# Performance work log

Hardware: AMD Instinct MI355X
Metric: run time of the kernel (lower is better)

## Reference

```python
import jax, jax.numpy as jnp
import numpy as np

B, S, D, H = 2, 2048, 1024, 16
DH = D // H  # 64


def setup_inputs() -> dict:
    key = jax.random.key(0)
    ks = jax.random.split(key, 6)
    scale = 1.0 / np.sqrt(D)
    x = jax.random.normal(ks[0], (B, S, D), dtype=jnp.float32)
    Wq = jax.random.normal(ks[1], (D, D), dtype=jnp.float32) * scale
    Wk = jax.random.normal(ks[2], (D, D), dtype=jnp.float32) * scale
    Wv = jax.random.normal(ks[3], (D, D), dtype=jnp.float32) * scale
    Wo = jax.random.normal(ks[4], (D, D), dtype=jnp.float32) * scale
    zeros = jnp.zeros((D,), dtype=jnp.float32)
    return {"x": x, "Wq": Wq, "bq": zeros, "Wk": Wk, "bk": zeros,
            "Wv": Wv, "bv": zeros, "Wo": Wo, "bo": zeros}


def reference(x, Wq, bq, Wk, bk, Wv, bv, Wo, bo):
    # x: [B, S, D]
    def split_heads(t):
        # [B, S, D] -> [B, H, S, DH]
        return t.reshape(B, S, H, DH).transpose(0, 2, 1, 3)

    q = split_heads(x @ Wq + bq)
    k = split_heads(x @ Wk + bk)
    v = split_heads(x @ Wv + bv)

    scores = jnp.einsum('bhqd,bhkd->bhqk', q, k) / jnp.sqrt(jnp.float32(DH))
    weights = jax.nn.softmax(scores, axis=-1)          # [B, H, S, S]
    o = jnp.einsum('bhqk,bhkd->bhqd', weights, v)       # [B, H, S, DH]
    o = o.transpose(0, 2, 1, 3).reshape(B, S, D)        # merge heads
    return o @ Wo + bo
```

## Files before the change

### kernel.cpp

```cpp
#include <hip/hip_runtime.h>
#include <hip/hip_bf16.h>

#define DEV __device__ __forceinline__

typedef short bf16x8 __attribute__((ext_vector_type(8)));
typedef float f32x4 __attribute__((ext_vector_type(4)));
typedef unsigned int u32;

constexpr int BB = 2, SS = 2048, DD = 1024, HH = 16, DHD = 64;
constexpr int MM = BB * SS;
#define QSC 0.1803368801111f

#if __has_builtin(__builtin_amdgcn_exp2f)
#define EXP2(x) __builtin_amdgcn_exp2f(x)
#else
#define EXP2(x) exp2f(x)
#endif

DEV unsigned short f2bf(float f) {
    union { float f; unsigned int u; } v; v.f = f;
    return (unsigned short)((v.u + 0x8000u) >> 16);
}
#if __has_builtin(__builtin_amdgcn_perm)
DEV u32 pk2bf(float a, float b) {
    union { float f; u32 u; } ua, ub; ua.f = a; ub.f = b;
    return __builtin_amdgcn_perm(ub.u + 0x8000u, ua.u + 0x8000u, 0x07060302u);
}
#else
DEV u32 pk2bf(float a, float b) {
    union { float f; u32 u; } ua, ub; ua.f = a; ub.f = b;
    return ((ua.u + 0x8000u) >> 16) | ((ub.u + 0x8000u) & 0xffff0000u);
}
#endif

DEV bf16x8 ld_bf16x8(const unsigned short* p) { return *(const bf16x8*)p; }

DEV void gl16(const unsigned short* g, unsigned short* l) {
    __builtin_amdgcn_global_load_lds(
        (const __attribute__((address_space(1))) u32*)g,
        (__attribute__((address_space(3))) u32*)l, 16, 0, 0);
}

__global__ void prep(const float* __restrict__ x, unsigned short* __restrict__ xb,
                     const float* __restrict__ W0, const float* __restrict__ W1,
                     const float* __restrict__ W2, const float* __restrict__ W3,
                     unsigned short* __restrict__ WtBase) {
    __shared__ float tile[32][33];
    int blk = blockIdx.x;
    if (blk < 4096) {
        int i = blk * 256 + threadIdx.x;
        float4 v = ((const float4*)x)[i];
        uint2 o;
        o.x = pk2bf(v.x, v.y);
        o.y = pk2bf(v.z, v.w);
        ((uint2*)xb)[i] = o;
        return;
    }
    blk -= 4096;
    int wsel = blk >> 10;
    const float* W = (wsel == 0) ? W0 : (wsel == 1) ? W1 : (wsel == 2) ? W2 : W3;
    unsigned short* Wt = WtBase + (size_t)wsel * DD * DD;
    int t = blk & 1023;
    int n0 = (t & 31) * 32, k0 = (t >> 5) * 32;
    int tx = threadIdx.x & 31, ty = threadIdx.x >> 5;
    #pragma unroll
    for (int i = 0; i < 4; ++i)
        tile[ty + 8 * i][tx] = W[(size_t)(k0 + ty + 8 * i) * DD + n0 + tx];
    __syncthreads();
    #pragma unroll
    for (int i = 0; i < 4; ++i)
        Wt[(size_t)(n0 + ty + 8 * i) * DD + k0 + tx] = f2bf(tile[tx][ty + 8 * i]);
}

__global__ __launch_bounds__(256) void qkv_gemm(
    const unsigned short* __restrict__ xb,
    const unsigned short* __restrict__ WtBase,
    const float* __restrict__ bq, const float* __restrict__ bk, const float* __restrict__ bv,
    unsigned short* __restrict__ Qb, unsigned short* __restrict__ Kb, unsigned short* __restrict__ Vt)
{
    __shared__ __align__(16) unsigned short Ald[2][128 * 32];
    __shared__ __align__(16) unsigned short Bld[2][128 * 32];

    const int z = blockIdx.z;
    const unsigned short* Wt = WtBase + (size_t)z * DD * DD;
    const float* bias = (z == 0) ? bq : (z == 1) ? bk : bv;

    const int m0g = blockIdx.y * 128;
    const int n0g = blockIdx.x * 128;
    const int wave = threadIdx.x >> 6, lane = threadIdx.x & 63;
    const int quad = lane >> 4, lcol = lane & 15;
    const int mb = (wave & 1) * 64, nb = (wave >> 1) * 64;

    f32x4 acc[4][4];
    #pragma unroll
    for (int i = 0; i < 4; ++i)
        #pragma unroll
        for (int j = 0; j < 4; ++j) acc[i][j] = (f32x4){0.f, 0.f, 0.f, 0.f};

    auto stage = [&](int ks, int bf) {
        #pragma unroll
        for (int i = 0; i < 4; ++i) {
            int j = wave * 4 + i;
            if (j < 8) {
                int bi = j * 64 + lane;
                int row = bi >> 2, p = (bi & 3) ^ (row & 3);
                gl16(xb + (size_t)(m0g + row) * DD + ks + p * 8, &Ald[bf][j * 512]);
            } else {
                int jj = j - 8;
                int bi = jj * 64 + lane;
                int row = bi >> 2, p = (bi & 3) ^ (row & 3);
                gl16(Wt + (size_t)(n0g + row) * DD + ks + p * 8, &Bld[bf][jj * 512]);
            }
        }
    };

    stage(0, 0);
    __syncthreads();

    for (int kk = 0; kk < 32; ++kk) {
        int bf = kk & 1;
        if (kk + 1 < 32) stage((kk + 1) * 32, (kk + 1) & 1);
        bf16x8 af[4], bfr[4];
        #pragma unroll
        for (int mt = 0; mt < 4; ++mt) {
            int row = mb + mt * 16 + lcol;
            af[mt] = ld_bf16x8(&Ald[bf][(row * 4 + (quad ^ (row & 3))) * 8]);
        }
        #pragma unroll
        for (int nt = 0; nt < 4; ++nt) {
            int row = nb + nt * 16 + lcol;
            bfr[nt] = ld_bf16x8(&Bld[bf][(row * 4 + (quad ^ (row & 3))) * 8]);
        }
        if (z < 2) {
            #pragma unroll
            for (int mt = 0; mt < 4; ++mt)
                #pragma unroll
                for (int nt = 0; nt < 4; ++nt)
                    acc[mt][nt] = __builtin_amdgcn_mfma_f32_16x16x32_bf16(bfr[nt], af[mt], acc[mt][nt], 0, 0, 0);
        } else {
            #pragma unroll
            for (int mt = 0; mt < 4; ++mt)
                #pragma unroll
                for (int nt = 0; nt < 4; ++nt)
                    acc[mt][nt] = __builtin_amdgcn_mfma_f32_16x16x32_bf16(af[mt], bfr[nt], acc[mt][nt], 0, 0, 0);
        }
        __syncthreads();
    }

    if (z < 2) {
        unsigned short* dst = (z == 0) ? Qb : Kb;
        const float sc = (z == 0) ? QSC : 1.0f;
        #pragma unroll
        for (int mt = 0; mt < 4; ++mt)
            #pragma unroll
            for (int nt = 0; nt < 4; ++nt) {
                int m = m0g + mb + mt * 16 + lcol;
                int nbt = n0g + nb + nt * 16 + quad * 4;
                int b = m >> 11, s = m & (SS - 1);
                int h = nbt >> 6, dh0 = nbt & 63;
                float4 bv4 = *(const float4*)&bias[nbt];
                uint2 o;
                o.x = pk2bf((acc[mt][nt][0] + bv4.x) * sc, (acc[mt][nt][1] + bv4.y) * sc);
                o.y = pk2bf((acc[mt][nt][2] + bv4.z) * sc, (acc[mt][nt][3] + bv4.w) * sc);
                *(uint2*)&dst[(((size_t)b * HH + h) * SS + s) * DHD + dh0] = o;
            }
    } else {
        #pragma unroll
        for (int mt = 0; mt < 4; ++mt)
            #pragma unroll
            for (int nt = 0; nt < 4; ++nt) {
                int n = n0g + nb + nt * 16 + lcol;
                int mbt = m0g + mb + mt * 16 + quad * 4;
                int h = n >> 6, dh = n & 63;
                int b = mbt >> 11, s0 = mbt & (SS - 1);
                float bvv = bias[n];
                uint2 o;
                o.x = pk2bf(acc[mt][nt][0] + bvv, acc[mt][nt][1] + bvv);
                o.y = pk2bf(acc[mt][nt][2] + bvv, acc[mt][nt][3] + bvv);
                *(uint2*)&Vt[(((size_t)b * HH + h) * DHD + dh) * SS + s0] = o;
            }
    }
}

__global__ __launch_bounds__(512, 4) void attn(
    const unsigned short* __restrict__ Qb,
    const unsigned short* __restrict__ Kb,
    const unsigned short* __restrict__ Vt,
    unsigned short* __restrict__ Ob)
{
    __shared__ __align__(16) unsigned short Kld[2][64 * 64];
    __shared__ __align__(16) unsigned short Vld[2][64 * 64];
    __shared__ __align__(16) unsigned short tb[8][16 * 68];

    const int g = blockIdx.y * gridDim.x + blockIdx.x;
    const int bh = (g & 7) * 4 + ((g >> 3) & 3);
    const int qt = g >> 5;
    const int b = bh >> 4, h = bh & (HH - 1);
    const unsigned short* Qbh = Qb + (size_t)bh * SS * DHD;
    const unsigned short* Kbh = Kb + (size_t)bh * SS * DHD;
    const unsigned short* Vbh = Vt + (size_t)bh * DHD * SS;

    const int wave = threadIdx.x >> 6, lane = threadIdx.x & 63;
    const int quad = lane >> 4, lcol = lane & 15;
    const int rowbase = qt * 128 + wave * 16;

    bf16x8 qf0 = ld_bf16x8(Qbh + (size_t)(rowbase + lcol) * DHD + quad * 8);
    bf16x8 qf1 = ld_bf16x8(Qbh + (size_t)(rowbase + lcol) * DHD + 32 + quad * 8);

    auto stage = [&](int c, int bf) {
        int kb = c * 64;
        #pragma unroll
        for (int i = 0; i < 2; ++i) {
            int j = wave * 2 + i;
            if (j < 8) {
                int bi = j * 64 + lane;
                int r = bi >> 3, p = (bi & 7) ^ (r & 7);
                gl16(Kbh + (size_t)(kb + r) * DHD + p * 8, &Kld[bf][j * 512]);
            } else {
                int jj = j - 8;
                int bi = jj * 64 + lane;
                int dh = bi >> 3, p = (bi & 7) ^ (dh & 7);
                gl16(Vbh + (size_t)dh * SS + kb + p * 8, &Vld[bf][jj * 512]);
            }
        }
    };

    stage(0, 0);
    __syncthreads();

    float m0 = -1e30f;
    #pragma unroll
    for (int kt = 0; kt < 4; ++kt) {
        int r0 = kt * 16 + lcol;
        bf16x8 ka0 = ld_bf16x8(&Kld[0][(r0 * 8 + (quad ^ (r0 & 7))) * 8]);
        bf16x8 ka1 = ld_bf16x8(&Kld[0][(r0 * 8 + ((quad + 4) ^ (r0 & 7))) * 8]);
        f32x4 s = (f32x4){0.f, 0.f, 0.f, 0.f};
        s = __builtin_amdgcn_mfma_f32_16x16x32_bf16(ka0, qf0, s, 0, 0, 0);
        s = __builtin_amdgcn_mfma_f32_16x16x32_bf16(ka1, qf1, s, 0, 0, 0);
        #pragma unroll
        for (int r = 0; r < 4; ++r) m0 = fmaxf(m0, s[r]);
    }
    #pragma unroll
    for (int msk = 1; msk < 64; msk <<= 1) m0 = fmaxf(m0, __shfl_xor(m0, msk, 64));
    const f32x4 minit = (f32x4){-m0, -m0, -m0, -m0};

    f32x4 oacc[4];
    #pragma unroll
    for (int nt = 0; nt < 4; ++nt) oacc[nt] = (f32x4){0.f, 0.f, 0.f, 0.f};
    float ps = 0.f;

    for (int c = 0; c < 32; ++c) {
        int bf = c & 1;
        if (c + 1 < 32) stage(c + 1, (c + 1) & 1);

        #pragma unroll
        for (int kt = 0; kt < 4; ++kt) {
            int r0 = kt * 16 + lcol;
            bf16x8 ka0 = ld_bf16x8(&Kld[bf][(r0 * 8 + (quad ^ (r0 & 7))) * 8]);
            bf16x8 ka1 = ld_bf16x8(&Kld[bf][(r0 * 8 + ((quad + 4) ^ (r0 & 7))) * 8]);
            f32x4 s = minit;
            s = __builtin_amdgcn_mfma_f32_16x16x32_bf16(ka0, qf0, s, 0, 0, 0);
            s = __builtin_amdgcn_mfma_f32_16x16x32_bf16(ka1, qf1, s, 0, 0, 0);
            float e0 = EXP2(s[0]), e1 = EXP2(s[1]);
            float e2 = EXP2(s[2]), e3 = EXP2(s[3]);
            ps += (e0 + e1) + (e2 + e3);
            *(uint2*)&tb[wave][lcol * 68 + kt * 16 + quad * 4] =
                make_uint2(pk2bf(e0, e1), pk2bf(e2, e3));
        }

        #pragma unroll
        for (int kf2 = 0; kf2 < 2; ++kf2) {
            bf16x8 pa = *(const bf16x8*)&tb[wave][lcol * 68 + kf2 * 32 + quad * 8];
            #pragma unroll
            for (int nt = 0; nt < 4; ++nt) {
                int dh = nt * 16 + lcol;
                bf16x8 vb = ld_bf16x8(&Vld[bf][(dh * 8 + ((kf2 * 4 + quad) ^ (dh & 7))) * 8]);
                oacc[nt] = __builtin_amdgcn_mfma_f32_16x16x32_bf16(pa, vb, oacc[nt], 0, 0, 0);
            }
        }
        __syncthreads();
    }

    ps += __shfl_xor(ps, 16, 64);
    ps += __shfl_xor(ps, 32, 64);
    float inv = 1.0f / ps;
    #pragma unroll
    for (int r = 0; r < 4; ++r) {
        float iv = __shfl(inv, quad * 4 + r, 64);
        int srow = rowbase + quad * 4 + r;
        size_t base = (((size_t)b * SS + srow) * HH + h) * DHD;
        #pragma unroll
        for (int nt = 0; nt < 4; ++nt)
            Ob[base + nt * 16 + lcol] = f2bf(oacc[nt][r] * iv);
    }
}

__global__ __launch_bounds__(256) void out_gemm(
    const unsigned short* __restrict__ Ob,
    const unsigned short* __restrict__ Wto,
    const float* __restrict__ bo,
    float* __restrict__ out)
{
    __shared__ __align__(16) unsigned short Wld[2][128 * 64];
    __shared__ __align__(16) unsigned short Old[2][64 * 64];

    const int m0g = blockIdx.y * 64;
    const int n0g = blockIdx.x * 128;
    const int wave = threadIdx.x >> 6, lane = threadIdx.x & 63;
    const int quad = lane >> 4, lcol = lane & 15;
    const int nb = wave * 32;

    f32x4 acc[2][4];
    #pragma unroll
    for (int i = 0; i < 2; ++i)
        #pragma unroll
        for (int j = 0; j < 4; ++j) acc[i][j] = (f32x4){0.f, 0.f, 0.f, 0.f};

    auto stage = [&](int ks, int bf) {
        #pragma unroll
        for (int i = 0; i < 6; ++i) {
            int j = wave * 6 + i;
            if (j < 16) {
                int bi = j * 64 + lane;
                int r = bi >> 3, p = (bi & 7) ^ (r & 7);
                gl16(Wto + (size_t)(n0g + r) * DD + ks + p * 8, &Wld[bf][j * 512]);
            } else {
                int jj = j - 16;
                int bi = jj * 64 + lane;
                int r = bi >> 3, p = (bi & 7) ^ (r & 7);
                gl16(Ob + (size_t)(m0g + r) * DD + ks + p * 8, &Old[bf][jj * 512]);
            }
        }
    };

    stage(0, 0);
    __syncthreads();

    for (int kk = 0; kk < 16; ++kk) {
        int bf = kk & 1;
        if (kk + 1 < 16) stage((kk + 1) * 64, (kk + 1) & 1);
        #pragma unroll
        for (int kh = 0; kh < 2; ++kh) {
            bf16x8 wf[2], of[4];
            #pragma unroll
            for (int i = 0; i < 2; ++i) {
                int row = nb + i * 16 + lcol;
                wf[i] = ld_bf16x8(&Wld[bf][(row * 8 + ((kh * 4 + quad) ^ (row & 7))) * 8]);
            }
            #pragma unroll
            for (int j = 0; j < 4; ++j) {
                int row = j * 16 + lcol;
                of[j] = ld_bf16x8(&Old[bf][(row * 8 + ((kh * 4 + quad) ^ (row & 7))) * 8]);
            }
            #pragma unroll
            for (int i = 0; i < 2; ++i)
                #pragma unroll
                for (int j = 0; j < 4; ++j)
                    acc[i][j] = __builtin_amdgcn_mfma_f32_16x16x32_bf16(wf[i], of[j], acc[i][j], 0, 0, 0);
        }
        __syncthreads();
    }

    #pragma unroll
    for (int i = 0; i < 2; ++i) {
        int n4 = n0g + nb + i * 16 + quad * 4;
        float4 bv4 = *(const float4*)&bo[n4];
        #pragma unroll
        for (int j = 0; j < 4; ++j) {
            int token = m0g + j * 16 + lcol;
            float4 o;
            o.x = acc[i][j][0] + bv4.x;
            o.y = acc[i][j][1] + bv4.y;
            o.z = acc[i][j][2] + bv4.z;
            o.w = acc[i][j][3] + bv4.w;
            *(float4*)&out[(size_t)token * DD + n4] = o;
        }
    }
}

extern "C" void kernel_launch(void* const* d_in, const int* in_sizes, int n_in,
                              void* d_out, int out_size, void* d_ws, size_t ws_size,
                              hipStream_t stream)
{
    const float* x  = (const float*)d_in[0];
    const float* Wq = (const float*)d_in[1];
    const float* bq = (const float*)d_in[2];
    const float* Wk = (const float*)d_in[3];
    const float* bk = (const float*)d_in[4];
    const float* Wv = (const float*)d_in[5];
    const float* bv = (const float*)d_in[6];
    const float* Wo = (const float*)d_in[7];
    const float* bo = (const float*)d_in[8];
    float* out = (float*)d_out;

    unsigned short* ws = (unsigned short*)d_ws;
    unsigned short* Wt  = ws;
    unsigned short* Wto = Wt + 3 * (size_t)DD * DD;
    unsigned short* Qb  = Wt + 4 * (size_t)DD * DD;
    unsigned short* Kb  = Qb + (size_t)MM * DD;
    unsigned short* Vt  = Kb + (size_t)MM * DD;
    unsigned short* xb  = Vt + (size_t)MM * DD;
    unsigned short* Ob  = xb;

    prep<<<8192, 256, 0, stream>>>(x, xb, Wq, Wk, Wv, Wo, Wt);

    qkv_gemm<<<dim3(DD / 128, MM / 128, 3), 256, 0, stream>>>(xb, Wt, bq, bk, bv, Qb, Kb, Vt);

    attn<<<dim3(16, 32), 512, 0, stream>>>(Qb, Kb, Vt, Ob);

    out_gemm<<<dim3(DD / 128, MM / 64), 256, 0, stream>>>(Ob, Wto, bo, out);
}
```

Measured before the change: 204.3 us.

## Give each attention wave two query row groups to reuse K/V fragments

```diff
diff --git a/kernel.cpp b/kernel.cpp
--- a/kernel.cpp
+++ b/kernel.cpp
@@ -32,6 +32,12 @@
     return ((ua.u + 0x8000u) >> 16) | ((ub.u + 0x8000u) & 0xffff0000u);
 }
 #endif
+
+DEV u32 cvtpk2bf(float a, float b) {
+    u32 r;
+    asm("v_cvt_pk_bf16_f32 %0, %1, %2" : "=v"(r) : "v"(a), "v"(b));
+    return r;
+}
 
 DEV bf16x8 ld_bf16x8(const unsigned short* p) { return *(const bf16x8*)p; }
 
@@ -182,7 +188,7 @@
     }
 }
 
-__global__ __launch_bounds__(512, 4) void attn(
+__global__ __launch_bounds__(256) void attn(
     const unsigned short* __restrict__ Qb,
     const unsigned short* __restrict__ Kb,
     const unsigned short* __restrict__ Vt,
@@ -190,7 +196,7 @@
 {
     __shared__ __align__(16) unsigned short Kld[2][64 * 64];
     __shared__ __align__(16) unsigned short Vld[2][64 * 64];
-    __shared__ __align__(16) unsigned short tb[8][16 * 68];
+    __shared__ __align__(16) unsigned short tb[4][32 * 68];
 
     const int g = blockIdx.y * gridDim.x + blockIdx.x;
     const int bh = (g & 7) * 4 + ((g >> 3) & 3);
@@ -202,16 +208,20 @@
 
     const int wave = threadIdx.x >> 6, lane = threadIdx.x & 63;
     const int quad = lane >> 4, lcol = lane & 15;
-    const int rowbase = qt * 128 + wave * 16;
-
-    bf16x8 qf0 = ld_bf16x8(Qbh + (size_t)(rowbase + lcol) * DHD + quad * 8);
-    bf16x8 qf1 = ld_bf16x8(Qbh + (size_t)(rowbase + lcol) * DHD + 32 + quad * 8);
+    const int rowbase = qt * 128 + wave * 32;
+
+    bf16x8 qf0[2], qf1[2];
+    #pragma unroll
+    for (int gq = 0; gq < 2; ++gq) {
+        qf0[gq] = ld_bf16x8(Qbh + (size_t)(rowbase + gq * 16 + lcol) * DHD + quad * 8);
+        qf1[gq] = ld_bf16x8(Qbh + (size_t)(rowbase + gq * 16 + lcol) * DHD + 32 + quad * 8);
+    }
 
     auto stage = [&](int c, int bf) {
         int kb = c * 64;
         #pragma unroll
-        for (int i = 0; i < 2; ++i) {
-            int j = wave * 2 + i;
+        for (int i = 0; i < 4; ++i) {
+            int j = wave * 4 + i;
             if (j < 8) {
                 int bi = j * 64 + lane;
                 int r = bi >> 3, p = (bi & 7) ^ (r & 7);
@@ -234,20 +244,25 @@
         int r0 = kt * 16 + lcol;
         bf16x8 ka0 = ld_bf16x8(&Kld[0][(r0 * 8 + (quad ^ (r0 & 7))) * 8]);
         bf16x8 ka1 = ld_bf16x8(&Kld[0][(r0 * 8 + ((quad + 4) ^ (r0 & 7))) * 8]);
-        f32x4 s = (f32x4){0.f, 0.f, 0.f, 0.f};
-        s = __builtin_amdgcn_mfma_f32_16x16x32_bf16(ka0, qf0, s, 0, 0, 0);
-        s = __builtin_amdgcn_mfma_f32_16x16x32_bf16(ka1, qf1, s, 0, 0, 0);
-        #pragma unroll
-        for (int r = 0; r < 4; ++r) m0 = fmaxf(m0, s[r]);
+        #pragma unroll
+        for (int gq = 0; gq < 2; ++gq) {
+            f32x4 s = (f32x4){0.f, 0.f, 0.f, 0.f};
+            s = __builtin_amdgcn_mfma_f32_16x16x32_bf16(ka0, qf0[gq], s, 0, 0, 0);
+            s = __builtin_amdgcn_mfma_f32_16x16x32_bf16(ka1, qf1[gq], s, 0, 0, 0);
+            #pragma unroll
+            for (int r = 0; r < 4; ++r) m0 = fmaxf(m0, s[r]);
+        }
     }
     #pragma unroll
     for (int msk = 1; msk < 64; msk <<= 1) m0 = fmaxf(m0, __shfl_xor(m0, msk, 64));
     const f32x4 minit = (f32x4){-m0, -m0, -m0, -m0};
 
-    f32x4 oacc[4];
-    #pragma unroll
-    for (int nt = 0; nt < 4; ++nt) oacc[nt] = (f32x4){0.f, 0.f, 0.f, 0.f};
-    float ps = 0.f;
+    f32x4 oacc[2][4];
+    #pragma unroll
+    for (int gq = 0; gq < 2; ++gq)
+        #pragma unroll
+        for (int nt = 0; nt < 4; ++nt) oacc[gq][nt] = (f32x4){0.f, 0.f, 0.f, 0.f};
+    float ps0 = 0.f, ps1 = 0.f;
 
     for (int c = 0; c < 32; ++c) {
         int bf = c & 1;
@@ -258,40 +273,61 @@
             int r0 = kt * 16 + lcol;
             bf16x8 ka0 = ld_bf16x8(&Kld[bf][(r0 * 8 + (quad ^ (r0 & 7))) * 8]);
             bf16x8 ka1 = ld_bf16x8(&Kld[bf][(r0 * 8 + ((quad + 4) ^ (r0 & 7))) * 8]);
-            f32x4 s = minit;
-            s = __builtin_amdgcn_mfma_f32_16x16x32_bf16(ka0, qf0, s, 0, 0, 0);
-            s = __builtin_amdgcn_mfma_f32_16x16x32_bf16(ka1, qf1, s, 0, 0, 0);
-            float e0 = EXP2(s[0]), e1 = EXP2(s[1]);
-            float e2 = EXP2(s[2]), e3 = EXP2(s[3]);
-            ps += (e0 + e1) + (e2 + e3);
-            *(uint2*)&tb[wave][lcol * 68 + kt * 16 + quad * 4] =
-                make_uint2(pk2bf(e0, e1), pk2bf(e2, e3));
+            f32x4 s0 = minit, s1 = minit;
+            __builtin_amdgcn_s_setprio(1);
+            s0 = __builtin_amdgcn_mfma_f32_16x16x32_bf16(ka0, qf0[0], s0, 0, 0, 0);
+            s0 = __builtin_amdgcn_mfma_f32_16x16x32_bf16(ka1, qf1[0], s0, 0, 0, 0);
+            s1 = __builtin_amdgcn_mfma_f32_16x16x32_bf16(ka0, qf0[1], s1, 0, 0, 0);
+            s1 = __builtin_amdgcn_mfma_f32_16x16x32_bf16(ka1, qf1[1], s1, 0, 0, 0);
+            __builtin_amdgcn_s_setprio(0);
+            {
+                float e0 = EXP2(s0[0]), e1 = EXP2(s0[1]);
+                float e2 = EXP2(s0[2]), e3 = EXP2(s0[3]);
+                ps0 += (e0 + e1) + (e2 + e3);
+                *(uint2*)&tb[wave][lcol * 68 + kt * 16 + quad * 4] =
+                    make_uint2(cvtpk2bf(e0, e1), cvtpk2bf(e2, e3));
+            }
+            {
+                float e0 = EXP2(s1[0]), e1 = EXP2(s1[1]);
+                float e2 = EXP2(s1[2]), e3 = EXP2(s1[3]);
+                ps1 += (e0 + e1) + (e2 + e3);
+                *(uint2*)&tb[wave][(16 + lcol) * 68 + kt * 16 + quad * 4] =
+                    make_uint2(cvtpk2bf(e0, e1), cvtpk2bf(e2, e3));
+            }
         }
 
         #pragma unroll
         for (int kf2 = 0; kf2 < 2; ++kf2) {
-            bf16x8 pa = *(const bf16x8*)&tb[wave][lcol * 68 + kf2 * 32 + quad * 8];
+            bf16x8 pa0 = *(const bf16x8*)&tb[wave][lcol * 68 + kf2 * 32 + quad * 8];
+            bf16x8 pa1 = *(const bf16x8*)&tb[wave][(16 + lcol) * 68 + kf2 * 32 + quad * 8];
             #pragma unroll
             for (int nt = 0; nt < 4; ++nt) {
                 int dh = nt * 16 + lcol;
                 bf16x8 vb = ld_bf16x8(&Vld[bf][(dh * 8 + ((kf2 * 4 + quad) ^ (dh & 7))) * 8]);
-                oacc[nt] = __builtin_amdgcn_mfma_f32_16x16x32_bf16(pa, vb, oacc[nt], 0, 0, 0);
+                __builtin_amdgcn_s_setprio(1);
+                oacc[0][nt] = __builtin_amdgcn_mfma_f32_16x16x32_bf16(pa0, vb, oacc[0][nt], 0, 0, 0);
+                oacc[1][nt] = __builtin_amdgcn_mfma_f32_16x16x32_bf16(pa1, vb, oacc[1][nt], 0, 0, 0);
+                __builtin_amdgcn_s_setprio(0);
             }
         }
         __syncthreads();
     }
 
-    ps += __shfl_xor(ps, 16, 64);
-    ps += __shfl_xor(ps, 32, 64);
-    float inv = 1.0f / ps;
-    #pragma unroll
-    for (int r = 0; r < 4; ++r) {
-        float iv = __shfl(inv, quad * 4 + r, 64);
-        int srow = rowbase + quad * 4 + r;
-        size_t base = (((size_t)b * SS + srow) * HH + h) * DHD;
-        #pragma unroll
-        for (int nt = 0; nt < 4; ++nt)
-            Ob[base + nt * 16 + lcol] = f2bf(oacc[nt][r] * iv);
+    #pragma unroll
+    for (int gq = 0; gq < 2; ++gq) {
+        float ps = (gq == 0) ? ps0 : ps1;
+        ps += __shfl_xor(ps, 16, 64);
+        ps += __shfl_xor(ps, 32, 64);
+        float inv = 1.0f / ps;
+        #pragma unroll
+        for (int r = 0; r < 4; ++r) {
+            float iv = __shfl(inv, quad * 4 + r, 64);
+            int srow = rowbase + gq * 16 + quad * 4 + r;
+            size_t base = (((size_t)b * SS + srow) * HH + h) * DHD;
+            #pragma unroll
+            for (int nt = 0; nt < 4; ++nt)
+                Ob[base + nt * 16 + lcol] = f2bf(oacc[gq][nt][r] * iv);
+        }
     }
 }
 
@@ -406,7 +442,7 @@
 
     qkv_gemm<<<dim3(DD / 128, MM / 128, 3), 256, 0, stream>>>(xb, Wt, bq, bk, bv, Qb, Kb, Vt);
 
-    attn<<<dim3(16, 32), 512, 0, stream>>>(Qb, Kb, Vt, Ob);
+    attn<<<dim3(16, 32), 256, 0, stream>>>(Qb, Kb, Vt, Ob);
 
     out_gemm<<<dim3(DD / 128, MM / 64), 256, 0, stream>>>(Ob, Wto, bo, out);
 }
```

After: 208.8 us. +2.2%, slower.

## Switch attention to 32x32x16 MFMA with in-register P via permlane swap

Applied to the files above, without the earlier changes.

```diff
diff --git a/kernel.cpp b/kernel.cpp
--- a/kernel.cpp
+++ b/kernel.cpp
@@ -5,7 +5,9 @@
 
 typedef short bf16x8 __attribute__((ext_vector_type(8)));
 typedef float f32x4 __attribute__((ext_vector_type(4)));
+typedef float f32x16 __attribute__((ext_vector_type(16)));
 typedef unsigned int u32;
+typedef unsigned int u32x4 __attribute__((ext_vector_type(4)));
 
 constexpr int BB = 2, SS = 2048, DD = 1024, HH = 16, DHD = 64;
 constexpr int MM = BB * SS;
@@ -32,6 +34,16 @@
     return ((ua.u + 0x8000u) >> 16) | ((ub.u + 0x8000u) & 0xffff0000u);
 }
 #endif
+
+DEV u32 cvtpk2bf(float a, float b) {
+    u32 r;
+    asm("v_cvt_pk_bf16_f32 %0, %1, %2" : "=v"(r) : "v"(a), "v"(b));
+    return r;
+}
+
+DEV void plswap(u32& a, u32& b) {
+    asm("v_permlane32_swap_b32 %0, %1" : "+v"(a), "+v"(b));
+}
 
 DEV bf16x8 ld_bf16x8(const unsigned short* p) { return *(const bf16x8*)p; }
 
@@ -188,9 +200,9 @@
     const unsigned short* __restrict__ Vt,
     unsigned short* __restrict__ Ob)
 {
-    __shared__ __align__(16) unsigned short Kld[2][64 * 64];
-    __shared__ __align__(16) unsigned short Vld[2][64 * 64];
-    __shared__ __align__(16) unsigned short tb[8][16 * 68];
+    __shared__ __align__(16) unsigned short smem[2][2][64 * 64];
+    __shared__ float psw[8][32];
+    __shared__ float smax[8];
 
     const int g = blockIdx.y * gridDim.x + blockIdx.x;
     const int bh = (g & 7) * 4 + ((g >> 3) & 3);
@@ -201,11 +213,15 @@
     const unsigned short* Vbh = Vt + (size_t)bh * DHD * SS;
 
     const int wave = threadIdx.x >> 6, lane = threadIdx.x & 63;
-    const int quad = lane >> 4, lcol = lane & 15;
-    const int rowbase = qt * 128 + wave * 16;
-
-    bf16x8 qf0 = ld_bf16x8(Qbh + (size_t)(rowbase + lcol) * DHD + quad * 8);
-    bf16x8 qf1 = ld_bf16x8(Qbh + (size_t)(rowbase + lcol) * DHD + 32 + quad * 8);
+    const int l31 = lane & 31, lh = lane >> 5;
+    const int qg = wave >> 1, khalf = wave & 1;
+    const int rowbase = qt * 128 + qg * 32;
+    const int krow = khalf * 32 + l31;
+
+    bf16x8 qf[4];
+    #pragma unroll
+    for (int ks = 0; ks < 4; ++ks)
+        qf[ks] = ld_bf16x8(Qbh + (size_t)(rowbase + l31) * DHD + ks * 16 + lh * 8);
 
     auto stage = [&](int c, int bf) {
         int kb = c * 64;
@@ -215,83 +231,118 @@
             if (j < 8) {
                 int bi = j * 64 + lane;
                 int r = bi >> 3, p = (bi & 7) ^ (r & 7);
-                gl16(Kbh + (size_t)(kb + r) * DHD + p * 8, &Kld[bf][j * 512]);
+                gl16(Kbh + (size_t)(kb + r) * DHD + p * 8, &smem[bf][0][j * 512]);
             } else {
                 int jj = j - 8;
                 int bi = jj * 64 + lane;
                 int dh = bi >> 3, p = (bi & 7) ^ (dh & 7);
-                gl16(Vbh + (size_t)dh * SS + kb + p * 8, &Vld[bf][jj * 512]);
+                gl16(Vbh + (size_t)dh * SS + kb + p * 8, &smem[bf][1][jj * 512]);
             }
         }
     };
 
     stage(0, 0);
     __syncthreads();
-
-    float m0 = -1e30f;
-    #pragma unroll
-    for (int kt = 0; kt < 4; ++kt) {
-        int r0 = kt * 16 + lcol;
-        bf16x8 ka0 = ld_bf16x8(&Kld[0][(r0 * 8 + (quad ^ (r0 & 7))) * 8]);
-        bf16x8 ka1 = ld_bf16x8(&Kld[0][(r0 * 8 + ((quad + 4) ^ (r0 & 7))) * 8]);
-        f32x4 s = (f32x4){0.f, 0.f, 0.f, 0.f};
-        s = __builtin_amdgcn_mfma_f32_16x16x32_bf16(ka0, qf0, s, 0, 0, 0);
-        s = __builtin_amdgcn_mfma_f32_16x16x32_bf16(ka1, qf1, s, 0, 0, 0);
-        #pragma unroll
-        for (int r = 0; r < 4; ++r) m0 = fmaxf(m0, s[r]);
-    }
-    #pragma unroll
-    for (int msk = 1; msk < 64; msk <<= 1) m0 = fmaxf(m0, __shfl_xor(m0, msk, 64));
-    const f32x4 minit = (f32x4){-m0, -m0, -m0, -m0};
-
-    f32x4 oacc[4];
-    #pragma unroll
-    for (int nt = 0; nt < 4; ++nt) oacc[nt] = (f32x4){0.f, 0.f, 0.f, 0.f};
+    {
+        f32x16 a0;
+        #pragma unroll
+        for (int i = 0; i < 16; ++i) a0[i] = 0.f;
+        #pragma unroll
+        for (int ks = 0; ks < 4; ++ks) {
+            int p = ks * 2 + lh;
+            bf16x8 ka = ld_bf16x8(&smem[0][0][(krow * 8 + (p ^ (krow & 7))) * 8]);
+            a0 = __builtin_amdgcn_mfma_f32_32x32x16_bf16(ka, qf[ks], a0, 0, 0, 0);
+        }
+        float m0 = -1e30f;
+        #pragma unroll
+        for (int i = 0; i < 16; ++i) m0 = fmaxf(m0, a0[i]);
+        #pragma unroll
+        for (int msk = 1; msk < 64; msk <<= 1) m0 = fmaxf(m0, __shfl_xor(m0, msk, 64));
+        if (lane == 0) smax[wave] = m0;
+    }
+    __syncthreads();
+    float m0b = smax[0];
+    #pragma unroll
+    for (int w2 = 1; w2 < 8; ++w2) m0b = fmaxf(m0b, smax[w2]);
+    const float nm0 = -m0b;
+
+    f32x16 oacc[2];
+    #pragma unroll
+    for (int db = 0; db < 2; ++db)
+        #pragma unroll
+        for (int i = 0; i < 16; ++i) oacc[db][i] = 0.f;
     float ps = 0.f;
 
     for (int c = 0; c < 32; ++c) {
         int bf = c & 1;
         if (c + 1 < 32) stage(c + 1, (c + 1) & 1);
 
-        #pragma unroll
-        for (int kt = 0; kt < 4; ++kt) {
-            int r0 = kt * 16 + lcol;
-            bf16x8 ka0 = ld_bf16x8(&Kld[bf][(r0 * 8 + (quad ^ (r0 & 7))) * 8]);
-            bf16x8 ka1 = ld_bf16x8(&Kld[bf][(r0 * 8 + ((quad + 4) ^ (r0 & 7))) * 8]);
-            f32x4 s = minit;
-            s = __builtin_amdgcn_mfma_f32_16x16x32_bf16(ka0, qf0, s, 0, 0, 0);
-            s = __builtin_amdgcn_mfma_f32_16x16x32_bf16(ka1, qf1, s, 0, 0, 0);
-            float e0 = EXP2(s[0]), e1 = EXP2(s[1]);
-            float e2 = EXP2(s[2]), e3 = EXP2(s[3]);
-            ps += (e0 + e1) + (e2 + e3);
-            *(uint2*)&tb[wave][lcol * 68 + kt * 16 + quad * 4] =
-                make_uint2(pk2bf(e0, e1), pk2bf(e2, e3));
-        }
-
-        #pragma unroll
-        for (int kf2 = 0; kf2 < 2; ++kf2) {
-            bf16x8 pa = *(const bf16x8*)&tb[wave][lcol * 68 + kf2 * 32 + quad * 8];
-            #pragma unroll
-            for (int nt = 0; nt < 4; ++nt) {
-                int dh = nt * 16 + lcol;
-                bf16x8 vb = ld_bf16x8(&Vld[bf][(dh * 8 + ((kf2 * 4 + quad) ^ (dh & 7))) * 8]);
-                oacc[nt] = __builtin_amdgcn_mfma_f32_16x16x32_bf16(pa, vb, oacc[nt], 0, 0, 0);
-            }
-        }
+        f32x16 s;
+        #pragma unroll
+        for (int i = 0; i < 16; ++i) s[i] = nm0;
+        __builtin_amdgcn_s_setprio(1);
+        #pragma unroll
+        for (int ks = 0; ks < 4; ++ks) {
+            int p = ks * 2 + lh;
+            bf16x8 ka = ld_bf16x8(&smem[bf][0][(krow * 8 + (p ^ (krow & 7))) * 8]);
+            s = __builtin_amdgcn_mfma_f32_32x32x16_bf16(ka, qf[ks], s, 0, 0, 0);
+        }
+        __builtin_amdgcn_s_setprio(0);
+
+        u32 w[8];
+        float psl = 0.f;
+        #pragma unroll
+        for (int i = 0; i < 8; ++i) {
+            float ea = EXP2(s[2 * i]), eb = EXP2(s[2 * i + 1]);
+            psl += ea + eb;
+            w[i] = cvtpk2bf(ea, eb);
+        }
+        ps += psl;
+        plswap(w[0], w[2]); plswap(w[1], w[3]);
+        plswap(w[4], w[6]); plswap(w[5], w[7]);
+        union { u32x4 u; bf16x8 hv; } pa0, pa1;
+        pa0.u = (u32x4){w[0], w[1], w[2], w[3]};
+        pa1.u = (u32x4){w[4], w[5], w[6], w[7]};
+
+        __builtin_amdgcn_s_setprio(1);
+        #pragma unroll
+        for (int db = 0; db < 2; ++db) {
+            int dh = db * 32 + l31;
+            #pragma unroll
+            for (int ks2 = 0; ks2 < 2; ++ks2) {
+                int p = khalf * 4 + ks2 * 2 + lh;
+                bf16x8 vb = ld_bf16x8(&smem[bf][1][(dh * 8 + (p ^ (dh & 7))) * 8]);
+                oacc[db] = __builtin_amdgcn_mfma_f32_32x32x16_bf16(
+                    ks2 ? pa1.hv : pa0.hv, vb, oacc[db], 0, 0, 0);
+            }
+        }
+        __builtin_amdgcn_s_setprio(0);
         __syncthreads();
     }
 
-    ps += __shfl_xor(ps, 16, 64);
-    ps += __shfl_xor(ps, 32, 64);
-    float inv = 1.0f / ps;
-    #pragma unroll
-    for (int r = 0; r < 4; ++r) {
-        float iv = __shfl(inv, quad * 4 + r, 64);
-        int srow = rowbase + quad * 4 + r;
-        size_t base = (((size_t)b * SS + srow) * HH + h) * DHD;
-        #pragma unroll
-        for (int nt = 0; nt < 4; ++nt)
-            Ob[base + nt * 16 + lcol] = f2bf(oacc[nt][r] * iv);
+    float* exch = (float*)smem;
+    {
+        int other = khalf ^ 1;
+        #pragma unroll
+        for (int r = 0; r < 16; ++r) {
+            int q = (r & 3) + 8 * (r >> 2) + 4 * lh;
+            exch[wave * 1024 + q * 32 + l31] = oacc[other][r];
+        }
+        float ps2 = ps + __shfl_xor(ps, 32, 64);
+        if (lane < 32) psw[wave][lane] = ps2;
+    }
+    __syncthreads();
+    {
+        const float* po = &exch[(wave ^ 1) * 1024];
+        int dh = khalf * 32 + l31;
+        #pragma unroll
+        for (int r = 0; r < 16; ++r) {
+            int q = (r & 3) + 8 * (r >> 2) + 4 * lh;
+            float v = oacc[khalf][r] + po[q * 32 + l31];
+            float pst = psw[qg * 2][q] + psw[qg * 2 + 1][q];
+            int srow = rowbase + q;
+            Ob[(((size_t)b * SS + srow) * HH + h) * DHD + dh] = f2bf(v / pst);
+        }
     }
 }
 
```

Result: slower. 217.0 us (+6.2%).

## Keep softmax probabilities in registers via permuted K rows, drop LDS round-trip

Applied to the files above, without the earlier changes.

```diff
diff --git a/kernel.cpp b/kernel.cpp
--- a/kernel.cpp
+++ b/kernel.cpp
@@ -6,6 +6,7 @@
 typedef short bf16x8 __attribute__((ext_vector_type(8)));
 typedef float f32x4 __attribute__((ext_vector_type(4)));
 typedef unsigned int u32;
+typedef unsigned int u32x4 __attribute__((ext_vector_type(4)));
 
 constexpr int BB = 2, SS = 2048, DD = 1024, HH = 16, DHD = 64;
 constexpr int MM = BB * SS;
@@ -32,6 +33,12 @@
     return ((ua.u + 0x8000u) >> 16) | ((ub.u + 0x8000u) & 0xffff0000u);
 }
 #endif
+
+DEV u32 cvtpk2bf(float a, float b) {
+    u32 r;
+    asm("v_cvt_pk_bf16_f32 %0, %1, %2" : "=v"(r) : "v"(a), "v"(b));
+    return r;
+}
 
 DEV bf16x8 ld_bf16x8(const unsigned short* p) { return *(const bf16x8*)p; }
 
@@ -190,7 +197,6 @@
 {
     __shared__ __align__(16) unsigned short Kld[2][64 * 64];
     __shared__ __align__(16) unsigned short Vld[2][64 * 64];
-    __shared__ __align__(16) unsigned short tb[8][16 * 68];
 
     const int g = blockIdx.y * gridDim.x + blockIdx.x;
     const int bh = (g & 7) * 4 + ((g >> 3) & 3);
@@ -207,6 +213,11 @@
     bf16x8 qf0 = ld_bf16x8(Qbh + (size_t)(rowbase + lcol) * DHD + quad * 8);
     bf16x8 qf1 = ld_bf16x8(Qbh + (size_t)(rowbase + lcol) * DHD + 32 + quad * 8);
 
+    auto krow = [&](int kf2, int j) {
+        return kf2 * 32 + ((lcol >> 2) << 3) + j * 4 + (lcol & 3);
+    };
+    auto kswz = [](int r) { return (r & 3) | (((r >> 3) & 1) << 2); };
+
     auto stage = [&](int c, int bf) {
         int kb = c * 64;
         #pragma unroll
@@ -214,7 +225,7 @@
             int j = wave * 2 + i;
             if (j < 8) {
                 int bi = j * 64 + lane;
-                int r = bi >> 3, p = (bi & 7) ^ (r & 7);
+                int r = bi >> 3, p = (bi & 7) ^ ((r & 3) | (((r >> 3) & 1) << 2));
                 gl16(Kbh + (size_t)(kb + r) * DHD + p * 8, &Kld[bf][j * 512]);
             } else {
                 int jj = j - 8;
@@ -230,16 +241,18 @@
 
     float m0 = -1e30f;
     #pragma unroll
-    for (int kt = 0; kt < 4; ++kt) {
-        int r0 = kt * 16 + lcol;
-        bf16x8 ka0 = ld_bf16x8(&Kld[0][(r0 * 8 + (quad ^ (r0 & 7))) * 8]);
-        bf16x8 ka1 = ld_bf16x8(&Kld[0][(r0 * 8 + ((quad + 4) ^ (r0 & 7))) * 8]);
-        f32x4 s = (f32x4){0.f, 0.f, 0.f, 0.f};
-        s = __builtin_amdgcn_mfma_f32_16x16x32_bf16(ka0, qf0, s, 0, 0, 0);
-        s = __builtin_amdgcn_mfma_f32_16x16x32_bf16(ka1, qf1, s, 0, 0, 0);
-        #pragma unroll
-        for (int r = 0; r < 4; ++r) m0 = fmaxf(m0, s[r]);
-    }
+    for (int kf2 = 0; kf2 < 2; ++kf2)
+        #pragma unroll
+        for (int j = 0; j < 2; ++j) {
+            int kr = krow(kf2, j), sw = kswz(kr);
+            bf16x8 ka0 = ld_bf16x8(&Kld[0][(kr * 8 + (quad ^ sw)) * 8]);
+            bf16x8 ka1 = ld_bf16x8(&Kld[0][(kr * 8 + ((quad + 4) ^ sw)) * 8]);
+            f32x4 s = (f32x4){0.f, 0.f, 0.f, 0.f};
+            s = __builtin_amdgcn_mfma_f32_16x16x32_bf16(ka0, qf0, s, 0, 0, 0);
+            s = __builtin_amdgcn_mfma_f32_16x16x32_bf16(ka1, qf1, s, 0, 0, 0);
+            #pragma unroll
+            for (int r = 0; r < 4; ++r) m0 = fmaxf(m0, s[r]);
+        }
     #pragma unroll
     for (int msk = 1; msk < 64; msk <<= 1) m0 = fmaxf(m0, __shfl_xor(m0, msk, 64));
     const f32x4 minit = (f32x4){-m0, -m0, -m0, -m0};
@@ -253,29 +266,36 @@
         int bf = c & 1;
         if (c + 1 < 32) stage(c + 1, (c + 1) & 1);
 
-        #pragma unroll
-        for (int kt = 0; kt < 4; ++kt) {
-            int r0 = kt * 16 + lcol;
-            bf16x8 ka0 = ld_bf16x8(&Kld[bf][(r0 * 8 + (quad ^ (r0 & 7))) * 8]);
-            bf16x8 ka1 = ld_bf16x8(&Kld[bf][(r0 * 8 + ((quad + 4) ^ (r0 & 7))) * 8]);
-            f32x4 s = minit;
-            s = __builtin_amdgcn_mfma_f32_16x16x32_bf16(ka0, qf0, s, 0, 0, 0);
-            s = __builtin_amdgcn_mfma_f32_16x16x32_bf16(ka1, qf1, s, 0, 0, 0);
-            float e0 = EXP2(s[0]), e1 = EXP2(s[1]);
-            float e2 = EXP2(s[2]), e3 = EXP2(s[3]);
-            ps += (e0 + e1) + (e2 + e3);
-            *(uint2*)&tb[wave][lcol * 68 + kt * 16 + quad * 4] =
-                make_uint2(pk2bf(e0, e1), pk2bf(e2, e3));
-        }
-
+        bf16x8 paf[2];
         #pragma unroll
         for (int kf2 = 0; kf2 < 2; ++kf2) {
-            bf16x8 pa = *(const bf16x8*)&tb[wave][lcol * 68 + kf2 * 32 + quad * 8];
+            u32 w[4];
+            #pragma unroll
+            for (int j = 0; j < 2; ++j) {
+                int kr = krow(kf2, j), sw = kswz(kr);
+                bf16x8 ka0 = ld_bf16x8(&Kld[bf][(kr * 8 + (quad ^ sw)) * 8]);
+                bf16x8 ka1 = ld_bf16x8(&Kld[bf][(kr * 8 + ((quad + 4) ^ sw)) * 8]);
+                f32x4 s = minit;
+                s = __builtin_amdgcn_mfma_f32_16x16x32_bf16(ka0, qf0, s, 0, 0, 0);
+                s = __builtin_amdgcn_mfma_f32_16x16x32_bf16(ka1, qf1, s, 0, 0, 0);
+                float e0 = EXP2(s[0]), e1 = EXP2(s[1]);
+                float e2 = EXP2(s[2]), e3 = EXP2(s[3]);
+                ps += (e0 + e1) + (e2 + e3);
+                w[j * 2]     = cvtpk2bf(e0, e1);
+                w[j * 2 + 1] = cvtpk2bf(e2, e3);
+            }
+            union { u32x4 u; bf16x8 v; } pu;
+            pu.u = (u32x4){w[0], w[1], w[2], w[3]};
+            paf[kf2] = pu.v;
+        }
+
+        #pragma unroll
+        for (int kf2 = 0; kf2 < 2; ++kf2) {
             #pragma unroll
             for (int nt = 0; nt < 4; ++nt) {
                 int dh = nt * 16 + lcol;
                 bf16x8 vb = ld_bf16x8(&Vld[bf][(dh * 8 + ((kf2 * 4 + quad) ^ (dh & 7))) * 8]);
-                oacc[nt] = __builtin_amdgcn_mfma_f32_16x16x32_bf16(pa, vb, oacc[nt], 0, 0, 0);
+                oacc[nt] = __builtin_amdgcn_mfma_f32_16x16x32_bf16(paf[kf2], vb, oacc[nt], 0, 0, 0);
             }
         }
         __syncthreads();
```

Result: faster. 197.3 us (-3.4%).
